# Kernel optimization log

Hardware: AMD Instinct MI355X
Metric: run time of the kernel (lower is better)

Reference implementation:

```python
import jax, jax.numpy as jnp
import numpy as np

N_E = 1024
E_DIM = 256
BETA = 0.25


def setup_inputs() -> dict:
    key = jax.random.key(0)
    k1, k2 = jax.random.split(key)
    z = jax.random.normal(k1, (16, E_DIM, 64, 64), dtype=jnp.float32)
    # nn.Embedding weight initialized uniform(-1/n_e, 1/n_e)
    codebook = jax.random.uniform(k2, (N_E, E_DIM), dtype=jnp.float32,
                                  minval=-1.0 / N_E, maxval=1.0 / N_E)
    return {"z": z, "codebook": codebook}


def reference(z, codebook):
    B, C, H, W = z.shape
    zp = jnp.transpose(z, (0, 2, 3, 1))              # [B,H,W,C]
    zf = zp.reshape(-1, C)                           # [N, e_dim]
    d = (jnp.sum(zf * zf, axis=1, keepdims=True)
         + jnp.sum(codebook * codebook, axis=1)
         - 2.0 * zf @ codebook.T)                    # [N, n_e]
    idx = jnp.argmin(d, axis=1)                      # [N]
    # one-hot @ codebook == direct gather
    z_q = codebook[idx].reshape(zp.shape)            # [B,H,W,C]

    e_latent_loss = jnp.mean((jax.lax.stop_gradient(z_q) - zp) ** 2)
    q_latent_loss = jnp.mean((z_q - jax.lax.stop_gradient(zp)) ** 2)
    codebook_loss = q_latent_loss + BETA * e_latent_loss

    # straight-through estimator
    z_q_st = zp + jax.lax.stop_gradient(z_q - zp)
    out = jnp.transpose(z_q_st, (0, 3, 1, 2))        # [B,C,H,W]
    indices = idx.reshape(B, 1, H, W)
    return out, codebook_loss, indices
```

## Files before the change

kernel.cpp:

```cpp
#include <hip/hip_runtime.h>

#define NB 16
#define NC 256
#define NH 64
#define NW 64
#define NK 1024
#define HW (NH * NW)
#define NPOS (NB * HW)
#define NOUT (NB * NC * HW)
#define NSLOT 256

__device__ __forceinline__ float sq_rn(float x) { return __fmul_rn(x, x); }

__device__ __forceinline__ float pairwise_sumsq_256(const float* __restrict__ a,
                                                    int stride) {
    float s_half[2];
#pragma unroll
    for (int h = 0; h < 2; ++h) {
        const float* base = a + (size_t)(h * 128) * stride;
        float r[8];
#pragma unroll
        for (int j = 0; j < 8; ++j) r[j] = sq_rn(base[(size_t)j * stride]);
        for (int i = 8; i < 128; i += 8) {
#pragma unroll
            for (int j = 0; j < 8; ++j)
                r[j] = __fadd_rn(r[j], sq_rn(base[(size_t)(i + j) * stride]));
        }
        s_half[h] = __fadd_rn(
            __fadd_rn(__fadd_rn(r[0], r[1]), __fadd_rn(r[2], r[3])),
            __fadd_rn(__fadd_rn(r[4], r[5]), __fadd_rn(r[6], r[7])));
    }
    return __fadd_rn(s_half[0], s_half[1]);
}

__global__ __launch_bounds__(256) void cnorm_kernel(const float* __restrict__ cb,
                                                    float* __restrict__ cnorm) {
    int k = blockIdx.x * 256 + threadIdx.x;
    if (k < NK) {
        cnorm[k] = pairwise_sumsq_256(cb + (size_t)k * NC, 1);
    }
}

__global__ __launch_bounds__(256) void pack_cb_kernel(const float* __restrict__ cb,
                                                      float* __restrict__ cbT2) {
    const int k = blockIdx.x;
    const int d = threadIdx.x;
    cbT2[(size_t)((d >> 2) * NK + k) * 4 + (d & 3)] = cb[(size_t)k * NC + d];
}

__global__ __launch_bounds__(512, 2) void argmin_kernel(const float* __restrict__ z,
                                                        const float* __restrict__ cb,
                                                        const float* __restrict__ cbT2,
                                                        const float* __restrict__ cnorm,
                                                        float* __restrict__ out,
                                                        float* __restrict__ idx_out,
                                                        double* __restrict__ loss_acc) {
    __shared__ float z_lds[256][64];
    __shared__ float znorm_s[64];
    __shared__ float red_v[8][64];
    __shared__ int   red_i[8][64];

    const int blk = blockIdx.x;
    const int b = blk >> 6;
    const int hw0 = (blk & 63) * 64;
    const int t = threadIdx.x;
    const int lane = t & 63;
    const int wave = t >> 6;
    const int pg = lane & 7;
    const int cg = lane >> 3;

    const float* zg = z + (size_t)b * (NC * HW) + hw0;

#pragma unroll
    for (int i = 0; i < 8; ++i) {
        const int flat4 = i * 2048 + t * 4;
        const int d = flat4 >> 6;
        const int p = flat4 & 63;
        const float4 v = *(const float4*)(zg + (size_t)d * HW + p);
        *(float4*)&z_lds[d][p] = v;
    }
    if (wave == 0) znorm_s[lane] = pairwise_sumsq_256(zg + lane, HW);
    __syncthreads();

    float best[8];
    int bid[8];
#pragma unroll
    for (int i = 0; i < 8; ++i) { best[i] = 3.4e38f; bid[i] = 0; }

#pragma unroll 1
    for (int pass = 0; pass < 2; ++pass) {
        float acc[8][8];
#pragma unroll
        for (int i = 0; i < 8; ++i)
#pragma unroll
            for (int j = 0; j < 8; ++j) acc[i][j] = 0.f;

        const int k0 = wave * 128 + pass * 64 + cg * 8;
        const float* cp2 = cbT2 + (size_t)k0 * 4;

#pragma unroll 1
        for (int it = 0; it < 64; ++it) {
            float4 cbuf[8];
#pragma unroll
            for (int q = 0; q < 8; ++q)
                cbuf[q] = *(const float4*)(cp2 + (size_t)it * 4096 + q * 4);
#pragma unroll
            for (int dl = 0; dl < 4; ++dl) {
                const int d = it * 4 + dl;
                const float4 za = *(const float4*)&z_lds[d][pg * 8];
                const float4 zb = *(const float4*)&z_lds[d][pg * 8 + 4];
                const float zf[8] = {za.x, za.y, za.z, za.w,
                                     zb.x, zb.y, zb.z, zb.w};
#pragma unroll
                for (int i = 0; i < 8; ++i)
#pragma unroll
                    for (int j = 0; j < 8; ++j)
                        acc[i][j] = __fmaf_rn(zf[i],
                                              ((const float*)&cbuf[j])[dl],
                                              acc[i][j]);
            }
        }

        const float4 cn0 = *(const float4*)(cnorm + k0);
        const float4 cn1 = *(const float4*)(cnorm + k0 + 4);
        const float cnf[8] = {cn0.x, cn0.y, cn0.z, cn0.w,
                              cn1.x, cn1.y, cn1.z, cn1.w};
        float znl[8];
#pragma unroll
        for (int i = 0; i < 8; ++i) znl[i] = znorm_s[pg * 8 + i];
#pragma unroll
        for (int j = 0; j < 8; ++j) {
            const int k = k0 + j;
#pragma unroll
            for (int i = 0; i < 8; ++i) {
                const float sc = __fsub_rn(__fadd_rn(znl[i], cnf[j]),
                                           __fmul_rn(2.0f, acc[i][j]));
                if (sc < best[i]) { best[i] = sc; bid[i] = k; }
            }
        }
    }

#pragma unroll
    for (int off = 32; off >= 8; off >>= 1) {
#pragma unroll
        for (int i = 0; i < 8; ++i) {
            const float v = __shfl_down(best[i], off, 64);
            const int d2 = __shfl_down(bid[i], off, 64);
            if (v < best[i] || (v == best[i] && d2 < bid[i])) {
                best[i] = v;
                bid[i] = d2;
            }
        }
    }
    if (cg == 0) {
#pragma unroll
        for (int i = 0; i < 8; ++i) {
            red_v[wave][pg * 8 + i] = best[i];
            red_i[wave][pg * 8 + i] = bid[i];
        }
    }
    __syncthreads();

    if (t < 64) {
        float bv = red_v[0][t];
        int bi = red_i[0][t];
#pragma unroll
        for (int w = 1; w < 8; ++w) {
            const float v = red_v[w][t];
            const int i2 = red_i[w][t];
            if (v < bv || (v == bv && i2 < bi)) { bv = v; bi = i2; }
        }
        idx_out[b * HW + hw0 + t] = (float)bi;
        red_i[0][t] = bi;
    }
    __syncthreads();

    float* outg = out + (size_t)b * (NC * HW) + hw0;
    float lsum = 0.f;
#pragma unroll 1
    for (int r = 0; r < 8; ++r) {
        const int id = r * 512 + t;
        const int c = id >> 4;
        const int p4 = (id & 15) * 4;
        const int i0 = red_i[0][p4];
        const int i1 = red_i[0][p4 + 1];
        const int i2 = red_i[0][p4 + 2];
        const int i3 = red_i[0][p4 + 3];
        float4 o;
        o.x = cb[(size_t)i0 * NC + c];
        o.y = cb[(size_t)i1 * NC + c];
        o.z = cb[(size_t)i2 * NC + c];
        o.w = cb[(size_t)i3 * NC + c];
        *(float4*)(outg + (size_t)c * HW + p4) = o;
        const float4 zv = *(const float4*)&z_lds[c][p4];
        const float d0 = o.x - zv.x;
        const float d1 = o.y - zv.y;
        const float d2 = o.z - zv.z;
        const float d3 = o.w - zv.w;
        lsum += d0 * d0 + d1 * d1 + d2 * d2 + d3 * d3;
    }
#pragma unroll
    for (int off = 32; off > 0; off >>= 1) lsum += __shfl_down(lsum, off, 64);
    if (lane == 0) red_v[wave][0] = lsum;
    __syncthreads();
    if (t == 0) {
        float s = 0.f;
#pragma unroll
        for (int w = 0; w < 8; ++w) s += red_v[w][0];
        atomicAdd(loss_acc + (blk & (NSLOT - 1)), (double)s);
    }
}

__global__ void finalize_kernel(const double* __restrict__ loss_acc,
                                float* __restrict__ out_loss) {
    if (threadIdx.x == 0) {
        double s = 0.0;
        for (int i = 0; i < NSLOT; ++i) s += loss_acc[i];
        *out_loss = (float)(1.25 * s / (double)NOUT);
    }
}

extern "C" void kernel_launch(void* const* d_in, const int* in_sizes, int n_in,
                              void* d_out, int out_size, void* d_ws, size_t ws_size,
                              hipStream_t stream) {
    const float* z = (const float*)d_in[0];
    const float* cb = (const float*)d_in[1];

    float* out = (float*)d_out;
    float* loss_out = out + NOUT;
    float* idx_out = out + NOUT + 1;

    double* loss_acc = (double*)d_ws;
    float* cnorm = (float*)((char*)d_ws + 2048);
    float* cbT2 = (float*)((char*)d_ws + 2048 + 4096);

    hipMemsetAsync(d_ws, 0, 2048, stream);
    cnorm_kernel<<<(NK + 255) / 256, 256, 0, stream>>>(cb, cnorm);
    pack_cb_kernel<<<NK, 256, 0, stream>>>(cb, cbT2);
    argmin_kernel<<<NPOS / 64, 512, 0, stream>>>(z, cb, cbT2, cnorm,
                                                 out, idx_out, loss_acc);
    finalize_kernel<<<1, 64, 0, stream>>>(loss_acc, loss_out);
}
```

Baseline: 580.3 us.

## Shrink argmin tile to 32 positions with 256 threads and repacked codebook layout

Retiles the distance/argmin kernel so each 256-thread block handles 32 spatial positions, with 4 waves each covering 256 codewords and 16 codeword groups per wave. The codebook is repacked so each lane's per-iteration float4 loads are spread across the wave for coalescing. The change doubles the block count and halves LDS per block to improve occupancy and load efficiency. In exchange, each codebook element is reused across fewer positions, so global/L2 traffic for the codebook doubles.

```diff
diff --git a/kernel.cpp b/kernel.cpp
--- a/kernel.cpp
+++ b/kernel.cpp
@@ -9,6 +9,7 @@
 #define NPOS (NB * HW)
 #define NOUT (NB * NC * HW)
 #define NSLOT 256
+#define TP 32
 
 __device__ __forceinline__ float sq_rn(float x) { return __fmul_rn(x, x); }
 
@@ -42,44 +43,48 @@
 }
 
 __global__ __launch_bounds__(256) void pack_cb_kernel(const float* __restrict__ cb,
-                                                      float* __restrict__ cbT2) {
+                                                      float* __restrict__ cbT3) {
     const int k = blockIdx.x;
     const int d = threadIdx.x;
-    cbT2[(size_t)((d >> 2) * NK + k) * 4 + (d & 3)] = cb[(size_t)k * NC + d];
-}
-
-__global__ __launch_bounds__(512, 2) void argmin_kernel(const float* __restrict__ z,
+    const int it = d >> 2, dl = d & 3;
+    const int kb = k >> 7;
+    const int q = k & 7;
+    const int cgi = (k >> 3) & 15;
+    cbT3[(size_t)(((it * 8 + kb) * 128) + q * 16 + cgi) * 4 + dl] =
+        cb[(size_t)k * NC + d];
+}
+
+__global__ __launch_bounds__(256, 2) void argmin_kernel(const float* __restrict__ z,
                                                         const float* __restrict__ cb,
-                                                        const float* __restrict__ cbT2,
+                                                        const float* __restrict__ cbT3,
                                                         const float* __restrict__ cnorm,
                                                         float* __restrict__ out,
                                                         float* __restrict__ idx_out,
                                                         double* __restrict__ loss_acc) {
-    __shared__ float z_lds[256][64];
-    __shared__ float znorm_s[64];
-    __shared__ float red_v[8][64];
-    __shared__ int   red_i[8][64];
+    __shared__ float z_lds[256][TP];
+    __shared__ float znorm_s[TP];
+    __shared__ float red_v[4][TP];
+    __shared__ int   red_i[4][TP];
 
     const int blk = blockIdx.x;
-    const int b = blk >> 6;
-    const int hw0 = (blk & 63) * 64;
+    const int b = blk >> 7;
+    const int hw0 = (blk & 127) * TP;
     const int t = threadIdx.x;
     const int lane = t & 63;
     const int wave = t >> 6;
-    const int pg = lane & 7;
-    const int cg = lane >> 3;
+    const int pg = lane >> 4;
+    const int cg = lane & 15;
 
     const float* zg = z + (size_t)b * (NC * HW) + hw0;
 
 #pragma unroll
     for (int i = 0; i < 8; ++i) {
-        const int flat4 = i * 2048 + t * 4;
-        const int d = flat4 >> 6;
-        const int p = flat4 & 63;
+        const int d = i * 32 + (t >> 3);
+        const int p = (t & 7) * 4;
         const float4 v = *(const float4*)(zg + (size_t)d * HW + p);
         *(float4*)&z_lds[d][p] = v;
     }
-    if (wave == 0) znorm_s[lane] = pairwise_sumsq_256(zg + lane, HW);
+    if (t < TP) znorm_s[t] = pairwise_sumsq_256(zg + t, HW);
     __syncthreads();
 
     float best[8];
@@ -95,15 +100,15 @@
 #pragma unroll
             for (int j = 0; j < 8; ++j) acc[i][j] = 0.f;
 
-        const int k0 = wave * 128 + pass * 64 + cg * 8;
-        const float* cp2 = cbT2 + (size_t)k0 * 4;
+        const int k0 = wave * 256 + pass * 128 + cg * 8;
+        const float* cp3 = cbT3 + (size_t)((wave * 2 + pass) * 512 + cg * 4);
 
 #pragma unroll 1
         for (int it = 0; it < 64; ++it) {
             float4 cbuf[8];
 #pragma unroll
             for (int q = 0; q < 8; ++q)
-                cbuf[q] = *(const float4*)(cp2 + (size_t)it * 4096 + q * 4);
+                cbuf[q] = *(const float4*)(cp3 + (size_t)it * 4096 + q * 64);
 #pragma unroll
             for (int dl = 0; dl < 4; ++dl) {
                 const int d = it * 4 + dl;
@@ -141,7 +146,7 @@
     }
 
 #pragma unroll
-    for (int off = 32; off >= 8; off >>= 1) {
+    for (int off = 8; off >= 1; off >>= 1) {
 #pragma unroll
         for (int i = 0; i < 8; ++i) {
             const float v = __shfl_down(best[i], off, 64);
@@ -161,11 +166,11 @@
     }
     __syncthreads();
 
-    if (t < 64) {
+    if (t < TP) {
         float bv = red_v[0][t];
         int bi = red_i[0][t];
 #pragma unroll
-        for (int w = 1; w < 8; ++w) {
+        for (int w = 1; w < 4; ++w) {
             const float v = red_v[w][t];
             const int i2 = red_i[w][t];
             if (v < bv || (v == bv && i2 < bi)) { bv = v; bi = i2; }
@@ -179,9 +184,9 @@
     float lsum = 0.f;
 #pragma unroll 1
     for (int r = 0; r < 8; ++r) {
-        const int id = r * 512 + t;
-        const int c = id >> 4;
-        const int p4 = (id & 15) * 4;
+        const int id = r * 256 + t;
+        const int c = id >> 3;
+        const int p4 = (id & 7) * 4;
         const int i0 = red_i[0][p4];
         const int i1 = red_i[0][p4 + 1];
         const int i2 = red_i[0][p4 + 2];
@@ -206,7 +211,7 @@
     if (t == 0) {
         float s = 0.f;
 #pragma unroll
-        for (int w = 0; w < 8; ++w) s += red_v[w][0];
+        for (int w = 0; w < 4; ++w) s += red_v[w][0];
         atomicAdd(loss_acc + (blk & (NSLOT - 1)), (double)s);
     }
 }
@@ -232,12 +237,12 @@
 
     double* loss_acc = (double*)d_ws;
     float* cnorm = (float*)((char*)d_ws + 2048);
-    float* cbT2 = (float*)((char*)d_ws + 2048 + 4096);
+    float* cbT3 = (float*)((char*)d_ws + 2048 + 4096);
 
     hipMemsetAsync(d_ws, 0, 2048, stream);
     cnorm_kernel<<<(NK + 255) / 256, 256, 0, stream>>>(cb, cnorm);
-    pack_cb_kernel<<<NK, 256, 0, stream>>>(cb, cbT2);
-    argmin_kernel<<<NPOS / 64, 512, 0, stream>>>(z, cb, cbT2, cnorm,
+    pack_cb_kernel<<<NK, 256, 0, stream>>>(cb, cbT3);
+    argmin_kernel<<<NPOS / TP, 256, 0, stream>>>(z, cb, cbT3, cnorm,
                                                  out, idx_out, loss_acc);
     finalize_kernel<<<1, 64, 0, stream>>>(loss_acc, loss_out);
 }
```

Result: faster. 543.6 us (-6.3%).
